# Kernel tuning notes

Measured on AMD Instinct MI355X. Metric: run time of the kernel, lower is better.

Reference implementation:

```python
import jax, jax.numpy as jnp
import numpy as np

D, K, B, IMG, NCH = 128, 512, 8, 128, 3


def adder2d(x, w, k, stride, pad):
    # AdderNet L1 'convolution': y[b,co,l] = -sum_p |patch[b,p,l] - w[co,p]|
    # x: [B,C,H,W], w: [Cout, C*k*k]
    p = jax.lax.conv_general_dilated_patches(x, (k, k), (stride, stride), [(pad, pad), (pad, pad)])
    Bb, P, Ho, Wo = p.shape
    p = p.reshape(Bb, P, Ho * Wo)  # [B, C*k*k, L]
    def one(wc):  # wc: [P] -> [B, L]; sequential over Cout to bound memory
        return -jnp.sum(jnp.abs(p - wc[None, :, None]), axis=1)
    o = jax.lax.map(one, w)  # [Cout, B, L]
    return jnp.transpose(o, (1, 0, 2)).reshape(Bb, w.shape[0], Ho, Wo)


def bn(x, g, b, eps=1e-5):
    # eval-mode BatchNorm2d with running_mean=0, running_var=1
    s = g * jax.lax.rsqrt(jnp.asarray(1.0 + eps, x.dtype))
    return x * s[None, :, None, None] + b[None, :, None, None]


def conv2d(x, w, b, pad):
    y = jax.lax.conv_general_dilated(x, w, (1, 1), [(pad, pad), (pad, pad)],
                                     dimension_numbers=('NCHW', 'OIHW', 'NCHW'))
    return y + b[None, :, None, None]


def up2x(x):  # nn.Upsample(scale_factor=2, bilinear, align_corners=False)
    Bb, C, H, W = x.shape
    return jax.image.resize(x, (Bb, C, 2 * H, 2 * W), method='bilinear')


def adder_resblock(x, w1, w2, g, b):
    # [ReLU, adder3x3, BN, ReLU, adder1x1] + residual
    h = jax.nn.relu(x)
    h = adder2d(h, w1, 3, 1, 1)
    h = bn(h, g, b)
    h = jax.nn.relu(h)
    h = adder2d(h, w2, 1, 1, 0)
    return x + h


def conv_resblock(x, w1, b1, w2, b2):
    # [ReLU, conv3x3, ReLU, conv1x1] + residual (bn=False in decoder)
    h = jax.nn.relu(x)
    h = conv2d(h, w1, b1, 1)
    h = jax.nn.relu(h)
    h = conv2d(h, w2, b2, 0)
    return x + h


def vq_forward(z_e, E):
    # NearestEmbed: E is [d, k]
    Bb, C, H, W = z_e.shape
    flat = jnp.transpose(z_e, (0, 2, 3, 1)).reshape(-1, C)  # [N, d]
    d2 = (jnp.sum(flat * flat, axis=1, keepdims=True)
          - 2.0 * (flat @ E) + jnp.sum(E * E, axis=0)[None, :])  # [N, k]
    argmin = jnp.argmin(d2, axis=1)  # [N]
    q = jnp.take(E.T, argmin, axis=0)  # [N, d]
    # weight_sg=True path: straight-through to z_e, no grad to E
    zq_flat = flat + jax.lax.stop_gradient(q - flat)
    z_q = jnp.transpose(zq_flat.reshape(Bb, H, W, C), (0, 3, 1, 2))
    # emb path: z_e detached, grad flows to E through the gather
    emb = jnp.transpose(q.reshape(Bb, H, W, C), (0, 3, 1, 2))
    return z_q, emb, argmin.reshape(Bb, H, W)


def reference(x, we1, we2, ae1_w1, ae1_w2, ae2_w1, ae2_w2, bn_gamma, bn_beta,
              emb_weight, rd1_w1, rd1_b1, rd1_w2, rd1_b2, rd2_w1, rd2_b1,
              rd2_w2, rd2_b2, cd1_w, cd1_b, cd2_w, cd2_b):
    g, b = bn_gamma, bn_beta
    h = adder2d(x, we1, 4, 2, 1)
    h = jax.nn.relu(bn(h, g[0], b[0]))
    h = adder2d(h, we2, 4, 2, 1)
    h = jax.nn.relu(bn(h, g[1], b[1]))
    h = adder_resblock(h, ae1_w1, ae1_w2, g[2], b[2])
    h = bn(h, g[3], b[3])
    h = adder_resblock(h, ae2_w1, ae2_w2, g[4], b[4])
    z_e = bn(h, g[5], b[5])  # bne4 (gamma = 1/40)

    z_q, emb, argmin = vq_forward(z_e, emb_weight)

    y = conv_resblock(z_q, rd1_w1, rd1_b1, rd1_w2, rd1_b2)
    y = bn(y, g[6], b[6])
    y = conv_resblock(y, rd2_w1, rd2_b1, rd2_w2, rd2_b2)
    y = up2x(y)
    y = conv2d(y, cd1_w, cd1_b, 1)
    y = jax.nn.relu(bn(y, g[7], b[7]))
    y = up2x(y)
    y = conv2d(y, cd2_w, cd2_b, 1)
    y = jnp.tanh(y)
    return (y, z_e, emb, argmin)


def setup_inputs() -> dict:
    key = jax.random.key(0)
    ks = jax.random.split(key, 16)
    f = lambda k, shp: (0.02 * jax.random.normal(k, shp)).astype(jnp.float32)
    inp = {}
    inp['x'] = jax.random.normal(ks[0], (B, NCH, IMG, IMG), jnp.float32)
    inp['we1'] = f(ks[1], (D, NCH * 16))       # adder 4x4 s2
    inp['we2'] = f(ks[2], (D, D * 16))
    inp['ae1_w1'] = f(ks[3], (D, D * 9))       # adder 3x3
    inp['ae1_w2'] = f(ks[4], (D, D))           # adder 1x1
    inp['ae2_w1'] = f(ks[5], (D, D * 9))
    inp['ae2_w2'] = f(ks[6], (D, D))
    inp['bn_gamma'] = jnp.ones((8, D), jnp.float32).at[5].set(1.0 / 40.0)
    inp['bn_beta'] = jnp.zeros((8, D), jnp.float32)
    inp['emb_weight'] = f(ks[7], (D, K))
    inp['rd1_w1'] = f(ks[8], (D, D, 3, 3)); inp['rd1_b1'] = jnp.zeros(D, jnp.float32)
    inp['rd1_w2'] = f(ks[9], (D, D, 1, 1)); inp['rd1_b2'] = jnp.zeros(D, jnp.float32)
    inp['rd2_w1'] = f(ks[10], (D, D, 3, 3)); inp['rd2_b1'] = jnp.zeros(D, jnp.float32)
    inp['rd2_w2'] = f(ks[11], (D, D, 1, 1)); inp['rd2_b2'] = jnp.zeros(D, jnp.float32)
    inp['cd1_w'] = f(ks[12], (D, D, 3, 3)); inp['cd1_b'] = jnp.zeros(D, jnp.float32)
    inp['cd2_w'] = f(ks[13], (NCH, D, 3, 3)); inp['cd2_b'] = jnp.zeros(NCH, jnp.float32)
    return inp
```

## Files before the change

kernel.cpp:

```cpp
#include <hip/hip_runtime.h>
#include <math.h>

constexpr int Dc = 128;
constexpr int Kc = 512;
constexpr int Bc = 8;

template<int ISADD, int K, int STRIDE, int PAD, int IT, int EPI, int CIN, int CH,
         int OUT_ROWS, int WOUT, int WIN, int HIN, int HOUT, int COBW>
__global__ __launch_bounds__(256)
void lds_layer(const float* __restrict__ x, const float* __restrict__ w,
               const float* __restrict__ bias,
               const float* __restrict__ itG, const float* __restrict__ itB,
               const float* __restrict__ res,
               const float* __restrict__ rG, const float* __restrict__ rB,
               const float* __restrict__ oG, const float* __restrict__ oB,
               float* __restrict__ out) {
  constexpr int PW = 2;
  constexpr int KK = K * K;
  constexpr int SPAN = (PW - 1) * STRIDE + K;
  constexpr int IN_ROWS = (OUT_ROWS - 1) * STRIDE + K;
  constexpr int WPAD = (WOUT - 1) * STRIDE + K;
  constexpr int WLDS = (WPAD + 3) & ~3;
  constexpr int PGW = WOUT / PW;
  static_assert(OUT_ROWS * PGW == 64, "one wave covers the pixel tile");
  constexpr int NCG = Dc / (4 * COBW);
  constexpr int NBAND = HOUT / OUT_ROWS;
  constexpr int W4 = WIN / 4;
  constexpr int NELEM4 = CH * IN_ROWS * W4;
  constexpr int NIT4 = (NELEM4 + 255) / 256;
  constexpr bool EXACT = (NELEM4 % 256) == 0;
  const float r15 = rsqrtf(1.0f + 1e-5f);

  __shared__ alignas(16) float lds[CH][IN_ROWS][WLDS];

  int tid = threadIdx.x;
  int gb = blockIdx.x;
  int cg = gb / (Bc * NBAND);
  int rem = gb % (Bc * NBAND);
  int band = rem % NBAND;
  int b = rem / NBAND;
  int wv = __builtin_amdgcn_readfirstlane(tid >> 6);
  int lane = tid & 63;
  int co0 = cg * (4 * COBW) + wv * COBW;
  int pr = lane / PGW, pc = lane % PGW;
  int oh = band * OUT_ROWS + pr;
  int ow0 = pc * PW;
  int yi0 = band * OUT_ROWS * STRIDE - PAD;

  for (int e = tid; e < CH * IN_ROWS * WLDS; e += 256) ((float*)lds)[e] = 0.f;

  float acc[PW][COBW];
#pragma unroll
  for (int p = 0; p < PW; ++p)
#pragma unroll
    for (int j = 0; j < COBW; ++j)
      acc[p][j] = ISADD ? 0.f : bias[co0 + j];

  const float* xb = x + (long)b * CIN * HIN * WIN;
  float4 rbuf[NIT4];

  auto stage = [&](int c0) {
#pragma unroll
    for (int it = 0; it < NIT4; ++it) {
      int e = it * 256 + tid;
      if (!EXACT && e >= NELEM4) break;
      int c4 = e % W4;
      int r = (e / W4) % IN_ROWS;
      int ch = e / (W4 * IN_ROWS);
      int yi = yi0 + r;
      float4 v = make_float4(0.f, 0.f, 0.f, 0.f);
      if (yi >= 0 && yi < HIN) {
        v = *(const float4*)&xb[((long)(c0 + ch) * HIN + yi) * WIN + 4 * c4];
        if (IT == 1) {
          v.x = fmaxf(v.x, 0.f); v.y = fmaxf(v.y, 0.f);
          v.z = fmaxf(v.z, 0.f); v.w = fmaxf(v.w, 0.f);
        }
        if (IT == 2) {
          float sc = itG[c0 + ch] * r15, bc = itB[c0 + ch];
          v.x = fmaxf(fmaf(v.x, sc, bc), 0.f);
          v.y = fmaxf(fmaf(v.y, sc, bc), 0.f);
          v.z = fmaxf(fmaf(v.z, sc, bc), 0.f);
          v.w = fmaxf(fmaf(v.w, sc, bc), 0.f);
        }
      }
      rbuf[it] = v;
    }
  };
  auto towrite = [&]() {
#pragma unroll
    for (int it = 0; it < NIT4; ++it) {
      int e = it * 256 + tid;
      if (!EXACT && e >= NELEM4) break;
      int c4 = e % W4;
      int r = (e / W4) % IN_ROWS;
      int ch = e / (W4 * IN_ROWS);
      float* p = &lds[ch][r][4 * c4 + PAD];
      float4 v = rbuf[it];
      p[0] = v.x; p[1] = v.y; p[2] = v.z; p[3] = v.w;
    }
  };

  stage(0);
  for (int c0 = 0; c0 < CIN; c0 += CH) {
    __syncthreads();
    towrite();
    __syncthreads();
    if (c0 + CH < CIN) stage(c0 + CH);
    for (int ch = 0; ch < CH; ++ch) {
      float vbuf[K][SPAN];
#pragma unroll
      for (int kh = 0; kh < K; ++kh) {
        const float* rp0 = &lds[ch][pr * STRIDE + kh][ow0 * STRIDE];
        if constexpr (SPAN == 6 && (PW * STRIDE) % 4 == 0) {
          float4 a = *(const float4*)rp0;
          float2 c2 = *(const float2*)(rp0 + 4);
          vbuf[kh][0] = a.x; vbuf[kh][1] = a.y; vbuf[kh][2] = a.z;
          vbuf[kh][3] = a.w; vbuf[kh][4] = c2.x; vbuf[kh][5] = c2.y;
        } else if constexpr (SPAN == 4 && (PW * STRIDE) % 2 == 0) {
          float2 a = *(const float2*)rp0;
          float2 c2 = *(const float2*)(rp0 + 2);
          vbuf[kh][0] = a.x; vbuf[kh][1] = a.y;
          vbuf[kh][2] = c2.x; vbuf[kh][3] = c2.y;
        } else if constexpr (SPAN == 2 && (PW * STRIDE) % 2 == 0) {
          float2 a = *(const float2*)rp0;
          vbuf[kh][0] = a.x; vbuf[kh][1] = a.y;
        } else {
#pragma unroll
          for (int s = 0; s < SPAN; ++s) vbuf[kh][s] = rp0[s];
        }
      }
      const float* wc = w + ((long)co0 * CIN + (c0 + ch)) * KK;
#pragma unroll
      for (int kh = 0; kh < K; ++kh)
#pragma unroll
        for (int kw = 0; kw < K; ++kw)
#pragma unroll
          for (int j = 0; j < COBW; ++j) {
            float ww = wc[(long)j * CIN * KK + kh * K + kw];
#pragma unroll
            for (int p = 0; p < PW; ++p) {
              float v = vbuf[kh][p * STRIDE + kw];
              if (ISADD) acc[p][j] += fabsf(v - ww);
              else       acc[p][j] = fmaf(v, ww, acc[p][j]);
            }
          }
    }
  }

  long obase = ((long)(b * Dc + co0) * HOUT + oh) * WOUT + ow0;
  float* ob = out + obase;
  const float* rp = (EPI == 2 || EPI == 3 || EPI == 6) ? res + obase : nullptr;
  constexpr long hw = (long)HOUT * WOUT;
#pragma unroll
  for (int j = 0; j < COBW; ++j) {
    float og = 0.f, obb = 0.f, rg = 0.f, rbb = 0.f;
    if (EPI == 1 || EPI == 6) { og = oG[co0 + j] * r15; obb = oB[co0 + j]; }
    if (EPI == 3 || EPI == 6) { rg = rG[co0 + j] * r15; rbb = rB[co0 + j]; }
#pragma unroll
    for (int p = 0; p < PW; ++p) {
      float val = ISADD ? -acc[p][j] : acc[p][j];
      if (EPI == 1) val = fmaxf(fmaf(val, og, obb), 0.f);
      if (EPI == 2) val = rp[j * hw + p] + val;
      if (EPI == 3) val = fmaf(rp[j * hw + p], rg, rbb) + val;
      if (EPI == 5) val = fmaxf(val, 0.f);
      if (EPI == 6) val = fmaf(fmaf(rp[j * hw + p], rg, rbb) + val, og, obb);
      ob[j * hw + p] = val;
    }
  }
}

__device__ __forceinline__ void up_coef(int p, int H, int& i0, int& i1, float& w0, float& w1) {
  int m = p >> 1;
  if ((p & 1) == 0) { i0 = (m > 0) ? m - 1 : 0; i1 = m; w0 = 0.25f; w1 = 0.75f; }
  else              { i0 = m; i1 = (m + 1 < H) ? m + 1 : H - 1; w0 = 0.75f; w1 = 0.25f; }
}

__global__ void up2x_kernel(const float* __restrict__ in, float* __restrict__ out,
                            int C, int H, int W) {
  int H2 = 2 * H, W2 = 2 * W;
  int i = blockIdx.x * blockDim.x + threadIdx.x;
  int total = Bc * C * H2 * W2;
  if (i >= total) return;
  int ow = i % W2; int t = i / W2;
  int oh = t % H2; t /= H2;
  int c = t % C; int b = t / C;
  int y0, y1, x0, x1; float wy0, wy1, wx0, wx1;
  up_coef(oh, H, y0, y1, wy0, wy1);
  up_coef(ow, W, x0, x1, wx0, wx1);
  const float* p = in + (b * C + c) * H * W;
  float v = wy0 * (wx0 * p[y0 * W + x0] + wx1 * p[y0 * W + x1])
          + wy1 * (wx0 * p[y1 * W + x0] + wx1 * p[y1 * W + x1]);
  out[i] = v;
}

__global__ __launch_bounds__(256)
void conv3x3_up_tanh_quad(const float* __restrict__ x, const float* __restrict__ w,
                          const float* __restrict__ bias, float* __restrict__ out,
                          int Hs, int Ws, int Cout) {
  constexpr int CIN = Dc;
  int H2 = 2 * Hs, W2 = 2 * Ws;
  int nq = Hs * Ws;
  int i = blockIdx.x * blockDim.x + threadIdx.x;
  int total = Bc * Cout * nq;
  if (i >= total) return;
  int q = i % nq; int t = i / nq;
  int co = t % Cout; int b = t / Cout;
  int n = q % Ws, m = q / Ws;
  int rows[3] = { (m > 0) ? m - 1 : 0, m, (m + 1 < Hs) ? m + 1 : Hs - 1 };
  int cols[3] = { (n > 0) ? n - 1 : 0, n, (n + 1 < Ws) ? n + 1 : Ws - 1 };
  float rv[4] = { (2 * m - 1 >= 0) ? 1.f : 0.f, 1.f, 1.f, (2 * m + 2 < H2) ? 1.f : 0.f };
  float cv[4] = { (2 * n - 1 >= 0) ? 1.f : 0.f, 1.f, 1.f, (2 * n + 2 < W2) ? 1.f : 0.f };
  float bco = bias[co];
  float acc[4] = { bco, bco, bco, bco };
  const float* xb = x + b * CIN * nq;
  const float* wb = w + co * CIN * 9;
  for (int c = 0; c < CIN; ++c) {
    const float* xc = xb + c * nq;
    float s[3][3];
#pragma unroll
    for (int a = 0; a < 3; ++a)
#pragma unroll
      for (int e = 0; e < 3; ++e) s[a][e] = xc[rows[a] * Ws + cols[e]];
    float rb[4][3];
#pragma unroll
    for (int e = 0; e < 3; ++e) {
      rb[0][e] = fmaf(0.75f, s[0][e], 0.25f * s[1][e]);
      rb[1][e] = fmaf(0.25f, s[0][e], 0.75f * s[1][e]);
      rb[2][e] = fmaf(0.75f, s[1][e], 0.25f * s[2][e]);
      rb[3][e] = fmaf(0.25f, s[1][e], 0.75f * s[2][e]);
    }
    float u[4][4];
#pragma unroll
    for (int di = 0; di < 4; ++di) {
      float rm = rv[di];
      u[di][0] = fmaf(0.75f, rb[di][0], 0.25f * rb[di][1]) * rm * cv[0];
      u[di][1] = fmaf(0.25f, rb[di][0], 0.75f * rb[di][1]) * rm * cv[1];
      u[di][2] = fmaf(0.75f, rb[di][1], 0.25f * rb[di][2]) * rm * cv[2];
      u[di][3] = fmaf(0.25f, rb[di][1], 0.75f * rb[di][2]) * rm * cv[3];
    }
    const float* wc = wb + c * 9;
#pragma unroll
    for (int kh = 0; kh < 3; ++kh)
#pragma unroll
      for (int kw = 0; kw < 3; ++kw) {
        float ww = wc[kh * 3 + kw];
        acc[0] = fmaf(u[kh][kw],         ww, acc[0]);
        acc[1] = fmaf(u[kh][kw + 1],     ww, acc[1]);
        acc[2] = fmaf(u[kh + 1][kw],     ww, acc[2]);
        acc[3] = fmaf(u[kh + 1][kw + 1], ww, acc[3]);
      }
  }
  float* ob = out + (b * Cout + co) * H2 * W2 + (2 * m) * W2 + 2 * n;
  ob[0] = tanhf(acc[0]);      ob[1] = tanhf(acc[1]);
  ob[W2] = tanhf(acc[2]);     ob[W2 + 1] = tanhf(acc[3]);
}

__global__ void vq_e2_kernel(const float* __restrict__ E, float* __restrict__ e2) {
  int k = blockIdx.x * blockDim.x + threadIdx.x;
  if (k >= Kc) return;
  float s = 0.f;
  for (int d = 0; d < Dc; ++d) { float v = E[d * Kc + k]; s += v * v; }
  e2[k] = s;
}

__global__ __launch_bounds__(256)
void vq_kernel8(const float* __restrict__ z_e, const float* __restrict__ E,
                const float* __restrict__ e2,
                float* __restrict__ emb, float* __restrict__ argmin_out) {
  constexpr int HW = 1024;
  __shared__ float f[8][Dc];
  __shared__ float d2s[8][256];
  __shared__ int   ks[8][256];
  int tid = threadIdx.x;
  int n0 = blockIdx.x * 8;
  int b = n0 >> 10;
  int rem = n0 & 1023;
  const float* zb = z_e + (long)b * Dc * HW + rem;
#pragma unroll
  for (int i = 0; i < 4; ++i) {
    int e = i * 256 + tid;
    int p = e & 7, d = e >> 3;
    f[p][d] = zb[d * HW + p];
  }
  __syncthreads();
  float f2 = 0.f;
  if (tid < 8) {
    for (int d = 0; d < Dc; ++d) f2 += f[tid][d] * f[tid][d];
    d2s[tid][0] = f2;
  }
  __syncthreads();
  float f2v[8];
#pragma unroll
  for (int p = 0; p < 8; ++p) f2v[p] = d2s[p][0];
  __syncthreads();

  float best[8]; int bk[8];
#pragma unroll
  for (int p = 0; p < 8; ++p) { best[p] = 3.4e38f; bk[p] = 0; }
  for (int kk = tid; kk < Kc; kk += 256) {
    float dot[8];
#pragma unroll
    for (int p = 0; p < 8; ++p) dot[p] = 0.f;
    for (int d = 0; d < Dc; ++d) {
      float ed = E[d * Kc + kk];
#pragma unroll
      for (int p = 0; p < 8; ++p) dot[p] = fmaf(f[p][d], ed, dot[p]);
    }
    float e2k = e2[kk];
#pragma unroll
    for (int p = 0; p < 8; ++p) {
      float d2 = f2v[p] - 2.f * dot[p] + e2k;
      if (d2 < best[p] || (d2 == best[p] && kk < bk[p])) { best[p] = d2; bk[p] = kk; }
    }
  }
#pragma unroll
  for (int p = 0; p < 8; ++p) { d2s[p][tid] = best[p]; ks[p][tid] = bk[p]; }
  __syncthreads();
  for (int s = 128; s > 0; s >>= 1) {
    if (tid < s) {
#pragma unroll
      for (int p = 0; p < 8; ++p) {
        float ob = d2s[p][tid + s]; int ok = ks[p][tid + s];
        if (ob < d2s[p][tid] || (ob == d2s[p][tid] && ok < ks[p][tid])) {
          d2s[p][tid] = ob; ks[p][tid] = ok;
        }
      }
    }
    __syncthreads();
  }
  if (tid < 8) argmin_out[n0 + tid] = (float)ks[tid][0];
  float* eb = emb + (long)b * Dc * HW + rem;
#pragma unroll
  for (int i = 0; i < 4; ++i) {
    int e = i * 256 + tid;
    int p = e & 7, d = e >> 3;
    eb[d * HW + p] = E[d * Kc + ks[p][0]];
  }
}

extern "C" void kernel_launch(void* const* d_in, const int* in_sizes, int n_in,
                              void* d_out, int out_size, void* d_ws, size_t ws_size,
                              hipStream_t stream) {
  const float* x      = (const float*)d_in[0];
  const float* we1    = (const float*)d_in[1];
  const float* we2    = (const float*)d_in[2];
  const float* ae1_w1 = (const float*)d_in[3];
  const float* ae1_w2 = (const float*)d_in[4];
  const float* ae2_w1 = (const float*)d_in[5];
  const float* ae2_w2 = (const float*)d_in[6];
  const float* bn_g   = (const float*)d_in[7];
  const float* bn_b   = (const float*)d_in[8];
  const float* embw   = (const float*)d_in[9];
  const float* rd1_w1 = (const float*)d_in[10];
  const float* rd1_b1 = (const float*)d_in[11];
  const float* rd1_w2 = (const float*)d_in[12];
  const float* rd1_b2 = (const float*)d_in[13];
  const float* rd2_w1 = (const float*)d_in[14];
  const float* rd2_b1 = (const float*)d_in[15];
  const float* rd2_w2 = (const float*)d_in[16];
  const float* rd2_b2 = (const float*)d_in[17];
  const float* cd1_w  = (const float*)d_in[18];
  const float* cd1_b  = (const float*)d_in[19];
  const float* cd2_w  = (const float*)d_in[20];
  const float* cd2_b  = (const float*)d_in[21];

  const float* g0 = bn_g + 0 * Dc; const float* b0 = bn_b + 0 * Dc;
  const float* g1 = bn_g + 1 * Dc; const float* b1 = bn_b + 1 * Dc;
  const float* g2 = bn_g + 2 * Dc; const float* b2 = bn_b + 2 * Dc;
  const float* g3 = bn_g + 3 * Dc; const float* b3 = bn_b + 3 * Dc;
  const float* g4 = bn_g + 4 * Dc; const float* b4 = bn_b + 4 * Dc;
  const float* g5 = bn_g + 5 * Dc; const float* b5 = bn_b + 5 * Dc;
  const float* g6 = bn_g + 6 * Dc; const float* b6 = bn_b + 6 * Dc;
  const float* g7 = bn_g + 7 * Dc; const float* b7 = bn_b + 7 * Dc;

  float* W64a = (float*)d_ws;
  float* W64b = W64a + 4194304;
  float* Wa   = W64b + 4194304;
  float* Wb   = Wa + 1048576;
  float* Wc   = Wb + 1048576;
  float* e2b  = W64b;

  float* out_y   = (float*)d_out;
  float* out_ze  = out_y  + 393216;
  float* out_emb = out_ze + 1048576;
  float* out_am  = out_emb + 1048576;

  const int TB = 256;
  auto nb = [](int n) { return (n + 255) / 256; };
  const int N64 = Bc * Dc * 64 * 64;
  const float* nul = nullptr;

  const int G32c2 = 16 * Bc * 8;
  const int G32c4 = 8 * Bc * 8;
  const int G64c4 = 8 * Bc * 32;
  const int G64c8 = 4 * Bc * 32;

  lds_layer<1,4,2,1, 0,1, 3,3, 2,64,128,128,64, 4><<<G64c4, TB, 0, stream>>>(
      x, we1, nul, nul, nul, nul, nul, nul, g0, b0, W64a);
  lds_layer<1,4,2,1, 0,1, Dc,8, 4,32,64,64,32, 2><<<G32c2, TB, 0, stream>>>(
      W64a, we2, nul, nul, nul, nul, nul, nul, g1, b1, Wa);
  lds_layer<1,3,1,1, 0,1, Dc,32, 4,32,32,32,32, 2><<<G32c2, TB, 0, stream>>>(
      Wa, ae1_w1, nul, nul, nul, nul, nul, nul, g2, b2, Wb);
  lds_layer<1,1,1,0, 0,2, Dc,64, 4,32,32,32,32, 4><<<G32c4, TB, 0, stream>>>(
      Wb, ae1_w2, nul, nul, nul, Wa, nul, nul, nul, nul, Wc);
  lds_layer<1,3,1,1, 2,1, Dc,32, 4,32,32,32,32, 2><<<G32c2, TB, 0, stream>>>(
      Wc, ae2_w1, nul, g3, b3, nul, nul, nul, g4, b4, Wb);
  lds_layer<1,1,1,0, 0,6, Dc,64, 4,32,32,32,32, 4><<<G32c4, TB, 0, stream>>>(
      Wb, ae2_w2, nul, nul, nul, Wc, g3, b3, g5, b5, out_ze);

  vq_e2_kernel<<<2, 256, 0, stream>>>(embw, e2b);
  vq_kernel8<<<Bc * 1024 / 8, 256, 0, stream>>>(out_ze, embw, e2b, out_emb, out_am);

  lds_layer<0,3,1,1, 1,5, Dc,32, 4,32,32,32,32, 2><<<G32c2, TB, 0, stream>>>(
      out_emb, rd1_w1, rd1_b1, nul, nul, nul, nul, nul, nul, nul, Wb);
  lds_layer<0,1,1,0, 0,2, Dc,64, 4,32,32,32,32, 4><<<G32c4, TB, 0, stream>>>(
      Wb, rd1_w2, rd1_b2, nul, nul, out_emb, nul, nul, nul, nul, Wa);
  lds_layer<0,3,1,1, 2,5, Dc,32, 4,32,32,32,32, 2><<<G32c2, TB, 0, stream>>>(
      Wa, rd2_w1, rd2_b1, g6, b6, nul, nul, nul, nul, nul, Wb);
  lds_layer<0,1,1,0, 0,3, Dc,64, 4,32,32,32,32, 4><<<G32c4, TB, 0, stream>>>(
      Wb, rd2_w2, rd2_b2, nul, nul, Wa, g6, b6, nul, nul, Wc);

  up2x_kernel<<<nb(N64), TB, 0, stream>>>(Wc, W64a, Dc, 32, 32);
  lds_layer<0,3,1,1, 0,1, Dc,16, 2,64,64,64,64, 8><<<G64c8, TB, 0, stream>>>(
      W64a, cd1_w, cd1_b, nul, nul, nul, nul, nul, g7, b7, W64b);

  conv3x3_up_tanh_quad<<<nb(Bc * 3 * 64 * 64), TB, 0, stream>>>(W64b, cd2_w, cd2_b, out_y, 64, 64, 3);
}
```

Before: 877.2 us.

## Repack weights into output-channel pairs and use packed 2-wide float math

Adds a repack kernel that interleaves weights of adjacent output channels so each layer can load a float2 per tap and accumulate with 2-wide vector ops (packed FMA, and for the adder layers a packed subtract, negate and max for the absolute difference). The aim is to halve the VALU instruction count and the scalar weight loads in the inner loops, relying on the compiler emitting packed-FP32 instructions. The cost is an extra repack launch on every call, plus workspace for the repacked weights. PW is now derived from the tile shape, but it evaluates to 2 for every instantiation.

```diff
diff --git a/kernel.cpp b/kernel.cpp
--- a/kernel.cpp
+++ b/kernel.cpp
@@ -5,17 +5,19 @@
 constexpr int Kc = 512;
 constexpr int Bc = 8;
 
+typedef float v2f __attribute__((ext_vector_type(2)));
+
 template<int ISADD, int K, int STRIDE, int PAD, int IT, int EPI, int CIN, int CH,
          int OUT_ROWS, int WOUT, int WIN, int HIN, int HOUT, int COBW>
 __global__ __launch_bounds__(256)
-void lds_layer(const float* __restrict__ x, const float* __restrict__ w,
+void lds_layer(const float* __restrict__ wp, const float* __restrict__ x,
                const float* __restrict__ bias,
                const float* __restrict__ itG, const float* __restrict__ itB,
                const float* __restrict__ res,
                const float* __restrict__ rG, const float* __restrict__ rB,
                const float* __restrict__ oG, const float* __restrict__ oB,
                float* __restrict__ out) {
-  constexpr int PW = 2;
+  constexpr int PW = (OUT_ROWS * WOUT) / 64;
   constexpr int KK = K * K;
   constexpr int SPAN = (PW - 1) * STRIDE + K;
   constexpr int IN_ROWS = (OUT_ROWS - 1) * STRIDE + K;
@@ -23,6 +25,8 @@
   constexpr int WLDS = (WPAD + 3) & ~3;
   constexpr int PGW = WOUT / PW;
   static_assert(OUT_ROWS * PGW == 64, "one wave covers the pixel tile");
+  static_assert((COBW & 1) == 0, "pk pairs need even COBW");
+  constexpr int JP = COBW / 2;
   constexpr int NCG = Dc / (4 * COBW);
   constexpr int NBAND = HOUT / OUT_ROWS;
   constexpr int W4 = WIN / 4;
@@ -49,12 +53,12 @@
 
   for (int e = tid; e < CH * IN_ROWS * WLDS; e += 256) ((float*)lds)[e] = 0.f;
 
-  float acc[PW][COBW];
+  v2f acc2[PW][JP];
 #pragma unroll
   for (int p = 0; p < PW; ++p)
 #pragma unroll
-    for (int j = 0; j < COBW; ++j)
-      acc[p][j] = ISADD ? 0.f : bias[co0 + j];
+    for (int jp = 0; jp < JP; ++jp)
+      acc2[p][jp] = ISADD ? (v2f){0.f, 0.f} : *(const v2f*)&bias[co0 + 2 * jp];
 
   const float* xb = x + (long)b * CIN * HIN * WIN;
   float4 rbuf[NIT4];
@@ -129,19 +133,24 @@
           for (int s = 0; s < SPAN; ++s) vbuf[kh][s] = rp0[s];
         }
       }
-      const float* wc = w + ((long)co0 * CIN + (c0 + ch)) * KK;
+      long wbase = (((long)(co0 >> 1) * CIN + (c0 + ch)) * KK) * 2;
 #pragma unroll
       for (int kh = 0; kh < K; ++kh)
 #pragma unroll
         for (int kw = 0; kw < K; ++kw)
 #pragma unroll
-          for (int j = 0; j < COBW; ++j) {
-            float ww = wc[(long)j * CIN * KK + kh * K + kw];
+          for (int jp = 0; jp < JP; ++jp) {
+            v2f w2 = *(const v2f*)&wp[wbase + (long)jp * CIN * KK * 2 + (kh * K + kw) * 2];
 #pragma unroll
             for (int p = 0; p < PW; ++p) {
               float v = vbuf[kh][p * STRIDE + kw];
-              if (ISADD) acc[p][j] += fabsf(v - ww);
-              else       acc[p][j] = fmaf(v, ww, acc[p][j]);
+              v2f vv = {v, v};
+              if (ISADD) {
+                v2f d = vv - w2;
+                acc2[p][jp] += __builtin_elementwise_max(d, -d);
+              } else {
+                acc2[p][jp] = __builtin_elementwise_fma(vv, w2, acc2[p][jp]);
+              }
             }
           }
     }
@@ -152,21 +161,42 @@
   const float* rp = (EPI == 2 || EPI == 3 || EPI == 6) ? res + obase : nullptr;
   constexpr long hw = (long)HOUT * WOUT;
 #pragma unroll
-  for (int j = 0; j < COBW; ++j) {
-    float og = 0.f, obb = 0.f, rg = 0.f, rbb = 0.f;
-    if (EPI == 1 || EPI == 6) { og = oG[co0 + j] * r15; obb = oB[co0 + j]; }
-    if (EPI == 3 || EPI == 6) { rg = rG[co0 + j] * r15; rbb = rB[co0 + j]; }
-#pragma unroll
-    for (int p = 0; p < PW; ++p) {
-      float val = ISADD ? -acc[p][j] : acc[p][j];
-      if (EPI == 1) val = fmaxf(fmaf(val, og, obb), 0.f);
-      if (EPI == 2) val = rp[j * hw + p] + val;
-      if (EPI == 3) val = fmaf(rp[j * hw + p], rg, rbb) + val;
-      if (EPI == 5) val = fmaxf(val, 0.f);
-      if (EPI == 6) val = fmaf(fmaf(rp[j * hw + p], rg, rbb) + val, og, obb);
-      ob[j * hw + p] = val;
-    }
-  }
+  for (int jp = 0; jp < JP; ++jp)
+#pragma unroll
+    for (int h = 0; h < 2; ++h) {
+      int j = 2 * jp + h;
+      float og = 0.f, obb = 0.f, rg = 0.f, rbb = 0.f;
+      if (EPI == 1 || EPI == 6) { og = oG[co0 + j] * r15; obb = oB[co0 + j]; }
+      if (EPI == 3 || EPI == 6) { rg = rG[co0 + j] * r15; rbb = rB[co0 + j]; }
+#pragma unroll
+      for (int p = 0; p < PW; ++p) {
+        float val = ISADD ? -acc2[p][jp][h] : acc2[p][jp][h];
+        if (EPI == 1) val = fmaxf(fmaf(val, og, obb), 0.f);
+        if (EPI == 2) val = rp[j * hw + p] + val;
+        if (EPI == 3) val = fmaf(rp[j * hw + p], rg, rbb) + val;
+        if (EPI == 5) val = fmaxf(val, 0.f);
+        if (EPI == 6) val = fmaf(fmaf(rp[j * hw + p], rg, rbb) + val, og, obb);
+        ob[j * hw + p] = val;
+      }
+    }
+}
+
+struct RepackDesc { const float* src; float* dst; int cinkk; int base; };
+struct RepackArgs { RepackDesc d[11]; int total; };
+
+__global__ void repack_k(RepackArgs a) {
+  int i = blockIdx.x * 256 + threadIdx.x;
+  if (i >= a.total) return;
+  int k = 0;
+#pragma unroll
+  for (int s = 1; s < 11; ++s) if (i >= a.d[s].base) k = s;
+  int local = i - a.d[k].base;
+  int cinkk = a.d[k].cinkk;
+  int t = local / cinkk, e = local % cinkk;
+  const float* src = a.d[k].src;
+  float* dst = a.d[k].dst;
+  dst[2 * local]     = src[(2 * t) * cinkk + e];
+  dst[2 * local + 1] = src[(2 * t + 1) * cinkk + e];
 }
 
 __device__ __forceinline__ void up_coef(int p, int H, int& i0, int& i1, float& w0, float& w1) {
@@ -378,6 +408,7 @@
   float* Wa   = W64b + 4194304;
   float* Wb   = Wa + 1048576;
   float* Wc   = Wb + 1048576;
+  float* WP   = Wc + 1048576;
   float* e2b  = W64b;
 
   float* out_y   = (float*)d_out;
@@ -390,39 +421,55 @@
   const int N64 = Bc * Dc * 64 * 64;
   const float* nul = nullptr;
 
+  const int cinkk[11] = { 48, 2048, 1152, 128, 1152, 128, 1152, 128, 1152, 128, 1152 };
+  const float* srcs[11] = { we1, we2, ae1_w1, ae1_w2, ae2_w1, ae2_w2,
+                            rd1_w1, rd1_w2, rd2_w1, rd2_w2, cd1_w };
+  RepackArgs ra;
+  int base = 0;
+  float* dst = WP;
+  float* wps[11];
+  for (int k = 0; k < 11; ++k) {
+    int pairs = 64 * cinkk[k];
+    ra.d[k].src = srcs[k]; ra.d[k].dst = dst; ra.d[k].cinkk = cinkk[k]; ra.d[k].base = base;
+    wps[k] = dst;
+    base += pairs; dst += 2 * pairs;
+  }
+  ra.total = base;
+  repack_k<<<nb(base), TB, 0, stream>>>(ra);
+
   const int G32c2 = 16 * Bc * 8;
   const int G32c4 = 8 * Bc * 8;
   const int G64c4 = 8 * Bc * 32;
   const int G64c8 = 4 * Bc * 32;
 
   lds_layer<1,4,2,1, 0,1, 3,3, 2,64,128,128,64, 4><<<G64c4, TB, 0, stream>>>(
-      x, we1, nul, nul, nul, nul, nul, nul, g0, b0, W64a);
+      wps[0], x, nul, nul, nul, nul, nul, nul, g0, b0, W64a);
   lds_layer<1,4,2,1, 0,1, Dc,8, 4,32,64,64,32, 2><<<G32c2, TB, 0, stream>>>(
-      W64a, we2, nul, nul, nul, nul, nul, nul, g1, b1, Wa);
+      wps[1], W64a, nul, nul, nul, nul, nul, nul, g1, b1, Wa);
   lds_layer<1,3,1,1, 0,1, Dc,32, 4,32,32,32,32, 2><<<G32c2, TB, 0, stream>>>(
-      Wa, ae1_w1, nul, nul, nul, nul, nul, nul, g2, b2, Wb);
+      wps[2], Wa, nul, nul, nul, nul, nul, nul, g2, b2, Wb);
   lds_layer<1,1,1,0, 0,2, Dc,64, 4,32,32,32,32, 4><<<G32c4, TB, 0, stream>>>(
-      Wb, ae1_w2, nul, nul, nul, Wa, nul, nul, nul, nul, Wc);
+      wps[3], Wb, nul, nul, nul, Wa, nul, nul, nul, nul, Wc);
   lds_layer<1,3,1,1, 2,1, Dc,32, 4,32,32,32,32, 2><<<G32c2, TB, 0, stream>>>(
-      Wc, ae2_w1, nul, g3, b3, nul, nul, nul, g4, b4, Wb);
+      wps[4], Wc, nul, g3, b3, nul, nul, nul, g4, b4, Wb);
   lds_layer<1,1,1,0, 0,6, Dc,64, 4,32,32,32,32, 4><<<G32c4, TB, 0, stream>>>(
-      Wb, ae2_w2, nul, nul, nul, Wc, g3, b3, g5, b5, out_ze);
+      wps[5], Wb, nul, nul, nul, Wc, g3, b3, g5, b5, out_ze);
 
   vq_e2_kernel<<<2, 256, 0, stream>>>(embw, e2b);
   vq_kernel8<<<Bc * 1024 / 8, 256, 0, stream>>>(out_ze, embw, e2b, out_emb, out_am);
 
   lds_layer<0,3,1,1, 1,5, Dc,32, 4,32,32,32,32, 2><<<G32c2, TB, 0, stream>>>(
-      out_emb, rd1_w1, rd1_b1, nul, nul, nul, nul, nul, nul, nul, Wb);
+      wps[6], out_emb, rd1_b1, nul, nul, nul, nul, nul, nul, nul, Wb);
   lds_layer<0,1,1,0, 0,2, Dc,64, 4,32,32,32,32, 4><<<G32c4, TB, 0, stream>>>(
-      Wb, rd1_w2, rd1_b2, nul, nul, out_emb, nul, nul, nul, nul, Wa);
+      wps[7], Wb, rd1_b2, nul, nul, out_emb, nul, nul, nul, nul, Wa);
   lds_layer<0,3,1,1, 2,5, Dc,32, 4,32,32,32,32, 2><<<G32c2, TB, 0, stream>>>(
-      Wa, rd2_w1, rd2_b1, g6, b6, nul, nul, nul, nul, nul, Wb);
+      wps[8], Wa, rd2_b1, g6, b6, nul, nul, nul, nul, nul, Wb);
   lds_layer<0,1,1,0, 0,3, Dc,64, 4,32,32,32,32, 4><<<G32c4, TB, 0, stream>>>(
-      Wb, rd2_w2, rd2_b2, nul, nul, Wa, g6, b6, nul, nul, Wc);
+      wps[9], Wb, rd2_b2, nul, nul, Wa, g6, b6, nul, nul, Wc);
 
   up2x_kernel<<<nb(N64), TB, 0, stream>>>(Wc, W64a, Dc, 32, 32);
   lds_layer<0,3,1,1, 0,1, Dc,16, 2,64,64,64,64, 8><<<G64c8, TB, 0, stream>>>(
-      W64a, cd1_w, cd1_b, nul, nul, nul, nul, nul, g7, b7, W64b);
+      wps[10], W64a, cd1_b, nul, nul, nul, nul, nul, g7, b7, W64b);
 
   conv3x3_up_tanh_quad<<<nb(Bc * 3 * 64 * 64), TB, 0, stream>>>(W64b, cd2_w, cd2_b, out_y, 64, 64, 3);
 }
```

Measured after the change: 938.7 us. 7.0% more time.
